# Performance work log

Measured on AMD Instinct MI355X. Metric: run time of the kernel, lower is better.

The kernel has to match this reference:

```python
import jax, jax.numpy as jnp
import numpy as np
from math import sqrt

FACTOR = 5

def setup_inputs() -> dict:
    key = jax.random.key(0)
    kq, kk, kv, ka = jax.random.split(key, 4)
    B, L, H, D = 4, 2048, 8, 64
    return {
        "queries": jax.random.normal(kq, (B, L, H, D), dtype=jnp.float32),
        "keys": jax.random.normal(kk, (B, L, H, D), dtype=jnp.float32),
        "values": jax.random.normal(kv, (B, L, H, D), dtype=jnp.float32),
        "atten_data": jax.random.normal(ka, (B, L, 2), dtype=jnp.float32),
        "attn_mask": jnp.zeros((1,), dtype=bool),  # unused (mask_flag=False)
    }

def reference(queries, keys, values, atten_data, attn_mask):
    # layer_num=1, mask_flag=False, output_attention=False, scale=None
    B, L_Q, H, D = queries.shape
    L_K = keys.shape[1]
    U_part = min(FACTOR * int(np.ceil(np.log(L_K))), L_K)  # sample_k
    u = min(FACTOR * int(np.ceil(np.log(L_Q))), L_Q)       # n_top

    Q = jnp.transpose(queries, (0, 2, 1, 3))  # [B,H,L_Q,D]
    K = jnp.transpose(keys, (0, 2, 1, 3))     # [B,H,L_K,D]
    V = jnp.transpose(values, (0, 2, 1, 3))   # [B,H,L_V,D]

    # --- _prob_QK: random K sampling per query position ---
    index_sample = jax.random.randint(jax.random.key(42), (L_Q, U_part), 0, L_K)
    K_sample = K[:, :, index_sample, :]                      # [B,H,L_Q,U_part,D]
    Q_K_sample = jnp.einsum("bhld,bhlsd->bhls", Q, K_sample)  # [B,H,L_Q,U_part]
    M = Q_K_sample.max(axis=-1) - Q_K_sample.sum(axis=-1) / L_K  # [B,H,L_Q]
    _, M_top = jax.lax.top_k(M, u)                           # [B,H,u]

    Q_reduce = jnp.take_along_axis(Q, M_top[..., None], axis=2)  # [B,H,u,D]
    scores_top = jnp.einsum("bhud,bhkd->bhuk", Q_reduce, K)      # [B,H,u,L_K]

    scale = 1.0 / sqrt(D)
    scores_top = scores_top * scale

    # --- initial context: mean of V broadcast over L_Q (mask_flag=False) ---
    V_mean = V.mean(axis=-2, keepdims=True)                  # [B,H,1,D]
    context = jnp.broadcast_to(V_mean, (B, H, L_Q, D))

    # --- update context at top-u query positions ---
    attn = jax.nn.softmax(scores_top, axis=-1)               # [B,H,u,L_K]
    upd = jnp.einsum("bhuk,bhkd->bhud", attn, V)             # [B,H,u,D]
    bidx = jnp.arange(B)[:, None, None]
    hidx = jnp.arange(H)[None, :, None]
    context = context.at[bidx, hidx, M_top].set(upd)

    return jnp.transpose(context, (0, 2, 1, 3))  # [B,L_Q,H,D]
```

## Files before the change

kernel.cpp:

```cpp
#include <hip/hip_runtime.h>
#include <math.h>

#define B_  4
#define L_  2048
#define H_  8
#define D_  64
#define U_  40
#define HD  (H_*D_)

#define WS_NEED_KC8 2937856

struct U2 { unsigned a, b; };

__host__ __device__ constexpr unsigned rotl32c(unsigned x, int r){
  return (x<<r)|(x>>(32-r));
}

__host__ __device__ constexpr U2 tf2x32(unsigned k0, unsigned k1,
                                        unsigned x0, unsigned x1)
{
  const unsigned k2 = k0 ^ k1 ^ 0x1BD11BDAu;
  const int rA[4] = {13,15,26,6};
  const int rB[4] = {17,29,16,24};
  x0 += k0; x1 += k1;
  for (int i=0;i<4;i++){ x0+=x1; x1=rotl32c(x1,rA[i]); x1^=x0; }
  x0 += k1; x1 += k2 + 1u;
  for (int i=0;i<4;i++){ x0+=x1; x1=rotl32c(x1,rB[i]); x1^=x0; }
  x0 += k2; x1 += k0 + 2u;
  for (int i=0;i<4;i++){ x0+=x1; x1=rotl32c(x1,rA[i]); x1^=x0; }
  x0 += k0; x1 += k1 + 3u;
  for (int i=0;i<4;i++){ x0+=x1; x1=rotl32c(x1,rB[i]); x1^=x0; }
  x0 += k1; x1 += k2 + 4u;
  for (int i=0;i<4;i++){ x0+=x1; x1=rotl32c(x1,rA[i]); x1^=x0; }
  x0 += k2; x1 += k0 + 5u;
  return U2{x0, x1};
}

__global__ __launch_bounds__(256) void mvm_kernel(const float* __restrict__ q,
                                                  const float* __restrict__ k,
                                                  const float* __restrict__ v,
                                                  float* __restrict__ M,
                                                  float* __restrict__ vmean)
{
  int tid = threadIdx.x;
  int w = tid >> 6, lane = tid & 63;

  if (blockIdx.x < 512){
    int g = blockIdx.x;
    int bh = g & 31, chunk = g >> 5;
    int b = bh >> 3, h = bh & 7;
    int l0 = chunk*128 + w*32;
    float s = 0.f;
    for (int i=0;i<32;i++)
      s += v[(size_t)(b*L_ + l0 + i)*HD + h*D_ + lane];
    atomicAdd(&vmean[bh*D_ + lane], s);
    return;
  }

  int g    = blockIdx.x - 512;
  int b    = g & 3;
  int lblk = g >> 2;
  int l    = lblk*4 + w;
  int h    = lane >> 3, d8 = lane & 7;

  const float* qrow = q + (size_t)(b*L_ + l)*HD;
  float4 q0 = *(const float4*)(qrow + lane*8);
  float4 q1 = *(const float4*)(qrow + lane*8 + 4);

  constexpr U2 K2 = tf2x32(0u, 42u, 0u, 1u);
  int myidx = 0;
  if (lane < U_){
    U2 r = tf2x32(K2.a, K2.b, 0u, (unsigned)(l*U_ + lane));
    myidx = (int)((r.a ^ r.b) & 2047u);
  }

  const float* kb = k + (size_t)b*L_*HD;
  float vmax = -INFINITY, vsum = 0.f;
  #pragma unroll 8
  for (int s=0;s<U_;s++){
    int kidx = __shfl(myidx, s, 64);
    const float* kr = kb + (size_t)kidx*HD;
    float4 k0 = *(const float4*)(kr + lane*8);
    float4 k1 = *(const float4*)(kr + lane*8 + 4);
    float p = q0.x*k0.x + q0.y*k0.y + q0.z*k0.z + q0.w*k0.w
            + q1.x*k1.x + q1.y*k1.y + q1.z*k1.z + q1.w*k1.w;
    p += __shfl_xor(p, 1, 64);
    p += __shfl_xor(p, 2, 64);
    p += __shfl_xor(p, 4, 64);
    vmax = fmaxf(vmax, p);
    vsum += p;
  }
  if (d8 == 0)
    M[(b*8 + h)*L_ + l] = vmax - vsum * (1.0f/(float)L_);
}

__global__ __launch_bounds__(256) void topk_init_kernel(const float* __restrict__ M,
                                                        const float* __restrict__ vmean,
                                                        int*   __restrict__ mtop,
                                                        float* __restrict__ out)
{
  int tid = threadIdx.x;

  if (blockIdx.x >= 32){
    int i = (blockIdx.x - 32)*256 + tid;
    int d4 = i & 15;
    int h  = (i >> 4) & 7;
    int bl = i >> 7;
    int b  = bl >> 11;
    float4 vm = ((const float4*)(vmean + (b*H_ + h)*D_))[d4];
    const float sc = 1.0f/(float)L_;
    float4 o; o.x = vm.x*sc; o.y = vm.y*sc; o.z = vm.z*sc; o.w = vm.w*sc;
    ((float4*)out)[i] = o;
    return;
  }

  __shared__ float mv[L_];
  __shared__ float bv[4];
  __shared__ int   bix[4];
  __shared__ int   wsh;
  int bh = blockIdx.x;
  int w = tid >> 6, lane = tid & 63;
  float tb = -INFINITY; int ti = tid;
  #pragma unroll
  for (int i=0;i<8;i++){
    float vv = M[bh*L_ + tid + 256*i];
    mv[tid + 256*i] = vv;
    if (vv > tb){ tb = vv; ti = tid + 256*i; }
  }
  for (int it=0; it<U_; ++it){
    float best = tb; int bi = ti;
    #pragma unroll
    for (int off=32; off; off>>=1){
      float ov = __shfl_xor(best, off, 64);
      int   oi = __shfl_xor(bi,   off, 64);
      if (ov > best || (ov == best && oi < bi)){ best = ov; bi = oi; }
    }
    if (lane == 0){ bv[w] = best; bix[w] = bi; }
    __syncthreads();
    if (tid == 0){
      float bb = bv[0]; int ii = bix[0];
      #pragma unroll
      for (int j=1;j<4;j++)
        if (bv[j] > bb || (bv[j] == bb && bix[j] < ii)){ bb = bv[j]; ii = bix[j]; }
      mtop[bh*U_ + it] = ii; wsh = ii;
    }
    __syncthreads();
    int wi = wsh;
    if (ti == wi){
      mv[wi] = -INFINITY;
      tb = -INFINITY; ti = tid;
      #pragma unroll
      for (int i=0;i<8;i++){
        float vv = mv[tid + 256*i];
        if (vv > tb){ tb = vv; ti = tid + 256*i; }
      }
    }
  }
}

__global__ __launch_bounds__(256, 3) void attn_kernel(const float* __restrict__ q,
                                                      const float* __restrict__ k,
                                                      const float* __restrict__ v,
                                                      const int*   __restrict__ mtop,
                                                      float* __restrict__ pacc,
                                                      float* __restrict__ pl,
                                                      int nt, int KC)
{
  __shared__ float sh[128*68 + 128*64 + 20*64];
  float* Kt  = sh;
  float* Vt  = sh + 128*68;
  float* Qs  = sh + 128*68 + 128*64;
  float* psQ = sh;

  int g  = blockIdx.x;
  int bh = g & 31, j = g >> 5;
  int kc = j >> 1, qg = j & 1;
  int b = bh >> 3, h = bh & 7;
  int tid = threadIdx.x, w = tid >> 6, lane = tid & 63;

  #pragma unroll
  for (int c=0;c<2;c++){
    int flat = c*256 + tid;
    if (flat < 320){
      int row = flat >> 4, col = flat & 15;
      int lstar = mtop[bh*U_ + qg*20 + row];
      ((float4*)(Qs + row*64))[col] =
        ((const float4*)(q + (size_t)(b*L_ + lstar)*HD + h*D_))[col];
    }
  }

  float acc[5], lsum[5];
  #pragma unroll
  for (int qq=0;qq<5;qq++){ acc[qq] = 0.f; lsum[qq] = 0.f; }

  for (int tt=0; tt<nt; ++tt){
    int kt = (kc*nt + tt)*128;
    __syncthreads();
    #pragma unroll
    for (int c=0;c<8;c++){
      int flat = c*256 + tid;
      int row = flat >> 4, col = flat & 15;
      ((float4*)(Kt + row*68))[col] =
        ((const float4*)(k + (size_t)(b*L_ + kt + row)*HD + h*D_))[col];
      ((float4*)(Vt + row*64))[col] =
        ((const float4*)(v + (size_t)(b*L_ + kt + row)*HD + h*D_))[col];
    }
    __syncthreads();

    float s0[5], s1[5];
    #pragma unroll
    for (int qq=0;qq<5;qq++){ s0[qq] = 0.f; s1[qq] = 0.f; }
    const float* kr0 = Kt + lane*68;
    const float* kr1 = Kt + (lane+64)*68;
    #pragma unroll
    for (int t=0;t<16;t++){
      float4 k0 = ((const float4*)kr0)[t];
      float4 k1 = ((const float4*)kr1)[t];
      #pragma unroll
      for (int qq=0;qq<5;qq++){
        float4 qf = ((const float4*)(Qs + (w*5+qq)*64))[t];
        s0[qq] += k0.x*qf.x + k0.y*qf.y + k0.z*qf.z + k0.w*qf.w;
        s1[qq] += k1.x*qf.x + k1.y*qf.y + k1.z*qf.z + k1.w*qf.w;
      }
    }
    __syncthreads();

    #pragma unroll
    for (int qq=0;qq<5;qq++){
      float p0 = __expf(s0[qq]*0.125f);
      float p1 = __expf(s1[qq]*0.125f);
      psQ[(w*5+qq)*128 + lane]      = p0;
      psQ[(w*5+qq)*128 + lane + 64] = p1;
      lsum[qq] += p0 + p1;
    }
    __syncthreads();

    for (int k4=0;k4<32;k4++){
      float v0 = Vt[(4*k4+0)*64 + lane];
      float v1 = Vt[(4*k4+1)*64 + lane];
      float v2 = Vt[(4*k4+2)*64 + lane];
      float v3 = Vt[(4*k4+3)*64 + lane];
      #pragma unroll
      for (int qq=0;qq<5;qq++){
        float4 pp = ((const float4*)(psQ + (w*5+qq)*128))[k4];
        acc[qq] += pp.x*v0 + pp.y*v1 + pp.z*v2 + pp.w*v3;
      }
    }
  }

  #pragma unroll
  for (int qq=0;qq<5;qq++){
    float ls = lsum[qq];
    #pragma unroll
    for (int off=32; off; off>>=1) ls += __shfl_xor(ls, off, 64);
    int gu = bh*U_ + qg*20 + w*5 + qq;
    pacc[(size_t)(gu*KC + kc)*64 + lane] = acc[qq];
    if (lane == 0) pl[gu*KC + kc] = ls;
  }
}

__global__ __launch_bounds__(256) void combine_kernel(const int* __restrict__ mtop,
                                                      const float* __restrict__ pacc,
                                                      const float* __restrict__ pl,
                                                      float* __restrict__ out,
                                                      int KC)
{
  int gu = blockIdx.x*4 + (threadIdx.x >> 6);
  int lane = threadIdx.x & 63;
  int bh = gu / U_, u = gu - bh*U_;
  float a = 0.f, L = 0.f;
  for (int c=0;c<KC;c++){
    a += pacc[(size_t)(gu*KC + c)*64 + lane];
    L += pl[gu*KC + c];
  }
  int b = bh >> 3, h = bh & 7;
  int lstar = mtop[bh*U_ + u];
  out[(size_t)(b*L_ + lstar)*HD + h*D_ + lane] = a / L;
}

extern "C" void kernel_launch(void* const* d_in, const int* in_sizes, int n_in,
                              void* d_out, int out_size, void* d_ws, size_t ws_size,
                              hipStream_t stream)
{
  const float* q = (const float*)d_in[0];
  const float* k = (const float*)d_in[1];
  const float* v = (const float*)d_in[2];
  float* out = (float*)d_out;

  int KC = (ws_size >= (size_t)WS_NEED_KC8) ? 8 : 4;
  int nt = 16 / KC;

  size_t o_pl    = (size_t)1280*KC*64*4;
  size_t o_vmean = o_pl + (size_t)1280*KC*4;
  size_t o_M     = o_vmean + 2048*4;
  size_t o_mtop  = o_M + 65536*4;

  float* pacc  = (float*)d_ws;
  float* pl    = (float*)((char*)d_ws + o_pl);
  float* vmean = (float*)((char*)d_ws + o_vmean);
  float* M     = (float*)((char*)d_ws + o_M);
  int*   mtop  = (int*)  ((char*)d_ws + o_mtop);

  hipMemsetAsync(vmean, 0, 2048*sizeof(float), stream);
  mvm_kernel      <<<2560,  256, 0, stream>>>(q, k, v, M, vmean);
  topk_init_kernel<<<4128,  256, 0, stream>>>(M, vmean, mtop, out);
  attn_kernel     <<<64*KC, 256, 0, stream>>>(q, k, v, mtop, pacc, pl, nt, KC);
  combine_kernel  <<<320,   256, 0, stream>>>(mtop, pacc, pl, out, KC);
}
```

Measured before the change: 189.4 us.

## Replace iterative argmax top-k with radix-select threshold and atomic scatter

The top-k selection over 2048 scores per (batch, head) used to run 40 rounds of block-wide argmax, each with two barriers. It now maps the floats to order-preserving unsigned keys and runs a 4-pass 8-bit radix select with shared-memory histograms to find the 40th-largest key. A final pass scatters qualifying indices through atomic counters. This cuts barrier-bound serial rounds, but the output order of indices becomes nondeterministic and ties are resolved differently, which matters only if downstream code depends on the order.

Measured after the change: 157.0 us. 17.1% less time.

```diff
diff --git a/kernel.cpp b/kernel.cpp
--- a/kernel.cpp
+++ b/kernel.cpp
@@ -114,46 +114,72 @@
     return;
   }
 
-  __shared__ float mv[L_];
-  __shared__ float bv[4];
-  __shared__ int   bix[4];
-  __shared__ int   wsh;
+  __shared__ unsigned keys[L_];
+  __shared__ unsigned hist[256];
+  __shared__ unsigned sh_prefix, sh_need, sh_cgt, sh_ceq;
   int bh = blockIdx.x;
-  int w = tid >> 6, lane = tid & 63;
-  float tb = -INFINITY; int ti = tid;
+
   #pragma unroll
   for (int i=0;i<8;i++){
-    float vv = M[bh*L_ + tid + 256*i];
-    mv[tid + 256*i] = vv;
-    if (vv > tb){ tb = vv; ti = tid + 256*i; }
-  }
-  for (int it=0; it<U_; ++it){
-    float best = tb; int bi = ti;
-    #pragma unroll
-    for (int off=32; off; off>>=1){
-      float ov = __shfl_xor(best, off, 64);
-      int   oi = __shfl_xor(bi,   off, 64);
-      if (ov > best || (ov == best && oi < bi)){ best = ov; bi = oi; }
-    }
-    if (lane == 0){ bv[w] = best; bix[w] = bi; }
-    __syncthreads();
-    if (tid == 0){
-      float bb = bv[0]; int ii = bix[0];
+    unsigned bits = __float_as_uint(M[bh*L_ + tid + 256*i]);
+    keys[tid + 256*i] = (bits & 0x80000000u) ? ~bits : (bits | 0x80000000u);
+  }
+  if (tid == 0){ sh_prefix = 0u; sh_need = U_; sh_cgt = 0u; sh_ceq = 0u; }
+
+  unsigned pmask = 0u;
+  for (int p = 3; p >= 0; --p){
+    hist[tid] = 0u;
+    __syncthreads();
+    unsigned pref = sh_prefix;
+    #pragma unroll
+    for (int i=0;i<8;i++){
+      unsigned key = keys[tid + 256*i];
+      if ((key & pmask) == pref)
+        atomicAdd(&hist[(key >> (8*p)) & 255u], 1u);
+    }
+    __syncthreads();
+
+    if (tid < 64){
+      unsigned h0 = hist[tid*4+0], h1 = hist[tid*4+1];
+      unsigned h2 = hist[tid*4+2], h3 = hist[tid*4+3];
+      unsigned loc = h0+h1+h2+h3;
+      unsigned s = loc;
       #pragma unroll
-      for (int j=1;j<4;j++)
-        if (bv[j] > bb || (bv[j] == bb && bix[j] < ii)){ bb = bv[j]; ii = bix[j]; }
-      mtop[bh*U_ + it] = ii; wsh = ii;
-    }
-    __syncthreads();
-    int wi = wsh;
-    if (ti == wi){
-      mv[wi] = -INFINITY;
-      tb = -INFINITY; ti = tid;
-      #pragma unroll
-      for (int i=0;i<8;i++){
-        float vv = mv[tid + 256*i];
-        if (vv > tb){ tb = vv; ti = tid + 256*i; }
+      for (int off=1; off<64; off<<=1){
+        unsigned o = __shfl_down(s, off, 64);
+        if (tid + off < 64) s += o;
       }
+      unsigned need = sh_need;
+      unsigned cum = s - loc;
+      unsigned bsel = 0xFFFFFFFFu, nn = 0u;
+      if (cum < need && cum + h3 >= need){ bsel = tid*4+3; nn = need - cum; }
+      cum += h3;
+      if (bsel==0xFFFFFFFFu && cum < need && cum + h2 >= need){ bsel = tid*4+2; nn = need - cum; }
+      cum += h2;
+      if (bsel==0xFFFFFFFFu && cum < need && cum + h1 >= need){ bsel = tid*4+1; nn = need - cum; }
+      cum += h1;
+      if (bsel==0xFFFFFFFFu && cum < need && cum + h0 >= need){ bsel = tid*4+0; nn = need - cum; }
+      if (bsel != 0xFFFFFFFFu){
+        sh_prefix = sh_prefix | (bsel << (8*p));
+        sh_need = nn;
+      }
+    }
+    __syncthreads();
+    pmask |= 0xFFu << (8*p);
+  }
+
+  unsigned K40 = sh_prefix;
+  unsigned need = sh_need;
+  #pragma unroll
+  for (int i=0;i<8;i++){
+    int idx = tid + 256*i;
+    unsigned key = keys[idx];
+    if (key > K40){
+      unsigned pos = atomicAdd(&sh_cgt, 1u);
+      mtop[bh*U_ + pos] = idx;
+    } else if (key == K40){
+      unsigned e = atomicAdd(&sh_ceq, 1u);
+      if (e < need) mtop[bh*U_ + (U_ - need) + e] = idx;
     }
   }
 }
```
